# Kernel tuning notes

Hardware: AMD Instinct MI355X
Metric: run time of the kernel (lower is better)

Reference implementation:

```python
import jax, jax.numpy as jnp
import numpy as np

VOCAB, EMBED, HID = 10, 256, 512
B, S, T = 8, 1024, 256  # Senc = S // 4 = 256


def _conv1d(x, w, b):
    # x: (B, Cin, L), w: (Cout, Cin, 3), padding=1 -> same length
    y = jax.lax.conv_general_dilated(x, w, window_strides=(1,), padding=[(1, 1)],
                                     dimension_numbers=('NCH', 'OIH', 'NCH'))
    return y + b[None, :, None]


def _maxpool2(x):
    # MaxPool1d(kernel=2, stride=2) on (B, C, L)
    b, c, l = x.shape
    return x.reshape(b, c, l // 2, 2).max(axis=-1)


def _lstm_layer(x, wih, whh, bih, bhh):
    # x: (B, T, Din); PyTorch gate order i, f, g, o; zero initial state
    b, t, _ = x.shape
    h_dim = whh.shape[1]
    xg = x @ wih.T + (bih + bhh)  # (B, T, 4H) - input projection hoisted out of scan

    def step(carry, xt):
        h, c = carry
        gates = xt + h @ whh.T
        i, f, g, o = jnp.split(gates, 4, axis=-1)
        c = jax.nn.sigmoid(f) * c + jax.nn.sigmoid(i) * jnp.tanh(g)
        h = jax.nn.sigmoid(o) * jnp.tanh(c)
        return (h, c), h

    init = (jnp.zeros((b, h_dim), x.dtype), jnp.zeros((b, h_dim), x.dtype))
    _, hs = jax.lax.scan(step, init, jnp.swapaxes(xg, 0, 1))
    return jnp.swapaxes(hs, 0, 1)  # (B, T, H)


def setup_inputs() -> dict:
    key = jax.random.key(0)
    ks = jax.random.split(key, 24)

    def unif(k, shape, fan_in):
        bound = 1.0 / np.sqrt(fan_in)
        return jax.random.uniform(k, shape, jnp.float32, -bound, bound)

    inp = {
        'src': jax.random.randint(ks[0], (B, S), 0, VOCAB),
        'tgt': jax.random.randint(ks[1], (B, T), 0, VOCAB),
        'embedding': jax.random.normal(ks[2], (VOCAB, EMBED), jnp.float32),
        'conv1_w': unif(ks[3], (256, EMBED, 3), EMBED * 3),
        'conv1_b': unif(ks[4], (256,), EMBED * 3),
        'conv2_w': unif(ks[5], (512, 256, 3), 256 * 3),
        'conv2_b': unif(ks[6], (512,), 256 * 3),
        'conv3_w': unif(ks[7], (512, 512, 3), 512 * 3),
        'conv3_b': unif(ks[8], (512,), 512 * 3),
        'lstm0_wih': unif(ks[9], (4 * HID, EMBED), HID),
        'lstm0_whh': unif(ks[10], (4 * HID, HID), HID),
        'lstm0_bih': unif(ks[11], (4 * HID,), HID),
        'lstm0_bhh': unif(ks[12], (4 * HID,), HID),
        'lstm1_wih': unif(ks[13], (4 * HID, HID), HID),
        'lstm1_whh': unif(ks[14], (4 * HID, HID), HID),
        'lstm1_bih': unif(ks[15], (4 * HID,), HID),
        'lstm1_bhh': unif(ks[16], (4 * HID,), HID),
        'attn_w': unif(ks[17], (1, 2 * HID), 2 * HID),
        'attn_b': unif(ks[18], (1,), 2 * HID),
        'out_w': unif(ks[19], (VOCAB, HID), HID),
        'out_b': unif(ks[20], (VOCAB,), HID),
    }
    return inp


def reference(src, tgt, embedding, conv1_w, conv1_b, conv2_w, conv2_b, conv3_w, conv3_b,
              lstm0_wih, lstm0_whh, lstm0_bih, lstm0_bhh,
              lstm1_wih, lstm1_whh, lstm1_bih, lstm1_bhh,
              attn_w, attn_b, out_w, out_b):
    # --- CNN encoder ---
    x = jnp.swapaxes(embedding[src], 1, 2)          # (B, E, S)
    x = _maxpool2(jax.nn.relu(_conv1d(x, conv1_w, conv1_b)))
    x = _maxpool2(jax.nn.relu(_conv1d(x, conv2_w, conv2_b)))
    x = jax.nn.relu(_conv1d(x, conv3_w, conv3_b))
    enc = jnp.swapaxes(x, 1, 2)                     # (B, Senc, 512)

    # --- LSTM decoder (2 layers) ---
    h = _lstm_layer(embedding[tgt], lstm0_wih, lstm0_whh, lstm0_bih, lstm0_bhh)
    dec = _lstm_layer(h, lstm1_wih, lstm1_whh, lstm1_bih, lstm1_bhh)  # (B, T, 512)

    # --- Bahdanau-style attention ---
    # Linear(cat([dec, enc])) == dec @ W[:, :H].T + enc @ W[:, H:].T + b,
    # so broadcast the two rank-1 projections instead of materializing (B,T,Senc,1024).
    dec_p = jnp.einsum('bth,h->bt', dec, attn_w[0, :HID])   # (B, T)
    enc_p = jnp.einsum('bsh,h->bs', enc, attn_w[0, HID:])   # (B, Senc)
    scores = dec_p[:, :, None] + enc_p[:, None, :] + attn_b[0]  # (B, T, Senc)
    attn = jax.nn.softmax(scores, axis=2)
    context = jnp.einsum('bts,bsd->btd', attn, enc)         # (B, T, 512)

    output = dec @ out_w.T + out_b                          # (B, T, VOCAB)
    # Original module computes context then discards it; we return it too so the
    # attention workload is not dead-code-eliminated under jit.
    return output, context
```

## Files before the change

kernel.cpp:

```cpp
#include <hip/hip_runtime.h>
#include <cstddef>

constexpr int OXB0 = 0;
constexpr int OXB1 = OXB0 + 8 * 1026 * 256;
constexpr int OXB2 = OXB1 + 8 * 514 * 256;
constexpr int OENC = OXB2 + 8 * 258 * 512;
constexpr int OWR1 = OENC + 8 * 256 * 512;
constexpr int OWR2 = OWR1 + 768 * 256;
constexpr int OWR3 = OWR2 + 768 * 512;
constexpr int OWR0 = OWR3 + 1536 * 512;
constexpr int OTGT = OWR0 + 256 * 2048;
constexpr int OXG0 = OTGT + 2048 * 256;
constexpr int OH0S = OXG0 + 2048 * 2048;
constexpr int OH1S = OH0S + 257 * 4096;
constexpr int OCTX = OH1S + 257 * 4096;
constexpr int OFLG = OCTX + 8 * 512;

constexpr int FSTR = 16;

__device__ __forceinline__ float hsum4(const float4& a) { return a.x + a.y + a.z + a.w; }
__device__ __forceinline__ float4 relu4(float4 v, const float4& bv) {
    v.x = fmaxf(v.x + bv.x, 0.f); v.y = fmaxf(v.y + bv.y, 0.f);
    v.z = fmaxf(v.z + bv.z, 0.f); v.w = fmaxf(v.w + bv.w, 0.f); return v;
}
__device__ __forceinline__ float4 max4(const float4& a, const float4& b) {
    float4 r; r.x = fmaxf(a.x, b.x); r.y = fmaxf(a.y, b.y);
    r.z = fmaxf(a.z, b.z); r.w = fmaxf(a.w, b.w); return r;
}
__device__ __forceinline__ float sigmf(float x) { return 1.f / (1.f + expf(-x)); }
__device__ __forceinline__ void fma4(float4& acc, const float4& a, const float4& b) {
    acc.x = fmaf(a.x, b.x, acc.x); acc.y = fmaf(a.y, b.y, acc.y);
    acc.z = fmaf(a.z, b.z, acc.z); acc.w = fmaf(a.w, b.w, acc.w);
}

__device__ __forceinline__ unsigned long long aload64(const float* p) {
    return __hip_atomic_load((const unsigned long long*)p, __ATOMIC_RELAXED,
                             __HIP_MEMORY_SCOPE_AGENT);
}
__device__ __forceinline__ void astore32(float* p, float v) {
    __hip_atomic_store((unsigned int*)p, __float_as_uint(v), __ATOMIC_RELAXED,
                       __HIP_MEMORY_SCOPE_AGENT);
}
__device__ __forceinline__ int aloadi(const int* p) {
    return __hip_atomic_load(p, __ATOMIC_RELAXED, __HIP_MEMORY_SCOPE_AGENT);
}
__device__ __forceinline__ void astorei(int* p, int v) {
    __hip_atomic_store(p, v, __ATOMIC_RELAXED, __HIP_MEMORY_SCOPE_AGENT);
}
__device__ __forceinline__ float2 unpack64(unsigned long long v) {
    float2 f;
    f.x = __uint_as_float((unsigned)v);
    f.y = __uint_as_float((unsigned)(v >> 32));
    return f;
}

__global__ void init_kernel(float* __restrict__ ws, int* __restrict__ flags) {
    int idx = blockIdx.x * 256 + threadIdx.x;
    int stride = gridDim.x * 256;
    for (int i = idx; i < 257 * 4096; i += stride) {
        ws[OH0S + i] = 0.f;
        ws[OH1S + i] = 0.f;
    }
    for (int i = idx; i < 192 * FSTR; i += stride) flags[i] = 0;
    for (int i = idx; i < 8 * 2 * 256; i += stride) {
        int b = i >> 9, rr = (i >> 8) & 1, c = i & 255;
        ws[OXB1 + b * 131584 + (rr ? 513 : 0) * 256 + c] = 0.f;
    }
    for (int i = idx; i < 8 * 2 * 512; i += stride) {
        int b = i >> 10, rr = (i >> 9) & 1, c = i & 511;
        ws[OXB2 + b * 132096 + (rr ? 257 : 0) * 512 + c] = 0.f;
    }
}

__global__ void embed_src_kernel(const int* __restrict__ src, const float* __restrict__ emb,
                                 float* __restrict__ xb0) {
    int fi = blockIdx.x * 256 + threadIdx.x;
    int e4 = fi & 63;
    int r = fi >> 6;
    int b = r / 1026;
    int p = r - b * 1026;
    float4 v = make_float4(0.f, 0.f, 0.f, 0.f);
    if (p > 0 && p < 1025) {
        int row = src[b * 1024 + (p - 1)];
        v = *(const float4*)(emb + row * 256 + e4 * 4);
    }
    *(float4*)(xb0 + (size_t)fi * 4) = v;
}

__global__ void gather_tgt_kernel(const int* __restrict__ tgt, const float* __restrict__ emb,
                                  float* __restrict__ et) {
    int fi = blockIdx.x * 256 + threadIdx.x;
    int e4 = fi & 63;
    int r = fi >> 6;
    int t = r >> 3, b = r & 7;
    int row = tgt[b * 256 + t];
    *(float4*)(et + (size_t)fi * 4) = *(const float4*)(emb + row * 256 + e4 * 4);
}

__global__ void tr_conv_kernel(const float* __restrict__ w, float* __restrict__ wr,
                               int Cout, int Cin) {
    int idx = blockIdx.x * 256 + threadIdx.x;
    int co = idx / (Cin * 3);
    int rem = idx - co * Cin * 3;
    int ci = rem / 3;
    int dk = rem - ci * 3;
    wr[(dk * Cin + ci) * Cout + co] = w[idx];
}
__global__ void tr_mat_kernel(const float* __restrict__ w, float* __restrict__ wr,
                              int N, int K) {
    int idx = blockIdx.x * 256 + threadIdx.x;
    int n = idx / K;
    int k = idx - n * K;
    wr[k * N + n] = w[idx];
}

__launch_bounds__(256)
// ... 37 lines not shown
            acc0.x = fmaf(a4.x, b4.x, acc0.x); acc0.y = fmaf(a4.x, b4.y, acc0.y);
            acc0.z = fmaf(a4.x, b4.z, acc0.z); acc0.w = fmaf(a4.x, b4.w, acc0.w);
            acc1.x = fmaf(a4.y, b4.x, acc1.x); acc1.y = fmaf(a4.y, b4.y, acc1.y);
            acc1.z = fmaf(a4.y, b4.z, acc1.z); acc1.w = fmaf(a4.y, b4.w, acc1.w);
            acc2.x = fmaf(a4.z, b4.x, acc2.x); acc2.y = fmaf(a4.z, b4.y, acc2.y);
            acc2.z = fmaf(a4.z, b4.z, acc2.z); acc2.w = fmaf(a4.z, b4.w, acc2.w);
            acc3.x = fmaf(a4.w, b4.x, acc3.x); acc3.y = fmaf(a4.w, b4.y, acc3.y);
            acc3.z = fmaf(a4.w, b4.z, acc3.z); acc3.w = fmaf(a4.w, b4.w, acc3.w);
        }
        __syncthreads();
    }

    int nb = n0 + tco * 4;
    float4 bv;
    bv.x = bias[nb + 0]; bv.y = bias[nb + 1]; bv.z = bias[nb + 2]; bv.w = bias[nb + 3];
    if (bias2) { bv.x += bias2[nb + 0]; bv.y += bias2[nb + 1]; bv.z += bias2[nb + 2]; bv.w += bias2[nb + 3]; }

    if (mode == 0) {
        float4 v0 = acc0, v1 = acc1, v2 = acc2, v3 = acc3;
        v0.x += bv.x; v0.y += bv.y; v0.z += bv.z; v0.w += bv.w;
        v1.x += bv.x; v1.y += bv.y; v1.z += bv.z; v1.w += bv.w;
        v2.x += bv.x; v2.y += bv.y; v2.z += bv.z; v2.w += bv.w;
        v3.x += bv.x; v3.y += bv.y; v3.z += bv.z; v3.w += bv.w;
        int mr = m0 + tl * 4;
        *(float4*)(out + (size_t)(mr + 0) * N + nb) = v0;
        *(float4*)(out + (size_t)(mr + 1) * N + nb) = v1;
        *(float4*)(out + (size_t)(mr + 2) * N + nb) = v2;
        *(float4*)(out + (size_t)(mr + 3) * N + nb) = v3;
    } else if (mode == 1) {
        float4 v0 = relu4(acc0, bv), v1 = relu4(acc1, bv), v2 = relu4(acc2, bv), v3 = relu4(acc3, bv);
        float4 p0 = max4(v0, v1), p1 = max4(v2, v3);
        int lout = (m0 + tl * 4) >> 1;
        float* ob = out + (size_t)b * oBS + (size_t)(1 + lout) * N + nb;
        *(float4*)ob = p0;
        *(float4*)(ob + N) = p1;
    } else {
        float4 v0 = relu4(acc0, bv), v1 = relu4(acc1, bv), v2 = relu4(acc2, bv), v3 = relu4(acc3, bv);
        int mr = m0 + tl * 4;
        float* ob = out + (size_t)b * oBS + (size_t)mr * N + nb;
        *(float4*)(ob + 0 * N) = v0;
        *(float4*)(ob + 1 * N) = v1;
        *(float4*)(ob + 2 * N) = v2;
        *(float4*)(ob + 3 * N) = v3;
    }
}

__launch_bounds__(256, 1)
__global__ void lstm_kernel(const float* __restrict__ xg0,
                            const float* __restrict__ whh0,
                            const float* __restrict__ wih1,
                            const float* __restrict__ whh1,
                            const float* __restrict__ bih1,
                            const float* __restrict__ bhh1,
                            float* __restrict__ h0s, float* __restrict__ h1s,
                            int* __restrict__ flags) {
    const int tid = threadIdx.x;
    const int wg = blockIdx.x;

    if (wg < 64) {
        const int wg0 = wg;
        const int cg = tid >> 6;
        const int bg = (tid >> 5) & 1;
        const int ks = tid & 31;
        float2 W2[4][2][8];
#pragma unroll
        for (int g = 0; g < 4; ++g)
#pragma unroll
            for (int e = 0; e < 2; ++e) {
                const float* wr = whh0 + (size_t)(g * 512 + wg0 * 8 + cg * 2 + e) * 512 + ks * 2;
#pragma unroll
                for (int q = 0; q < 8; ++q)
                    W2[g][e][q] = *(const float2*)(wr + q * 64);
            }
        const int vg = ks >> 3, ve = (ks >> 2) & 1, vbi = ks & 3;
        const int vb = bg * 4 + vbi;
        const size_t xgoff = (size_t)vb * 2048 + vg * 512 + wg0 * 8 + cg * 2 + ve;
        const int ob = bg * 4 + (ks & 3);
        const int ou = cg * 2 + ((ks >> 2) & 1);
        float cst = 0.f;

        for (int t = 0; t < 256; ++t) {
            float xgv = xg0[(size_t)t * 16384 + xgoff];
            if (t > 0 && tid < 64) {
                int gd = 1 << 20;
                while (aloadi(&flags[tid * FSTR]) < t && --gd) {}
            }
            __syncthreads();
            unsigned long long hv[4][8];
#pragma unroll
            for (int bi = 0; bi < 4; ++bi) {
                const float* hb = h0s + (size_t)t * 4096 + (bg * 4 + bi) * 512 + ks * 2;
#pragma unroll
                for (int q = 0; q < 8; ++q)
                    hv[bi][q] = aload64(hb + q * 64);
            }
            float2 acc[4][2][4];
#pragma unroll
            for (int g = 0; g < 4; ++g)
#pragma unroll
                for (int e = 0; e < 2; ++e)
#pragma unroll
                    for (int bi = 0; bi < 4; ++bi) acc[g][e][bi] = make_float2(0.f, 0.f);
#pragma unroll
            for (int q = 0; q < 8; ++q)
#pragma unroll
                for (int bi = 0; bi < 4; ++bi) {
                    float2 h2 = unpack64(hv[bi][q]);
#pragma unroll
                    for (int g = 0; g < 4; ++g)
#pragma unroll
                        for (int e = 0; e < 2; ++e) {
                            acc[g][e][bi].x = fmaf(W2[g][e][q].x, h2.x, acc[g][e][bi].x);
                            acc[g][e][bi].y = fmaf(W2[g][e][q].y, h2.y, acc[g][e][bi].y);
                        }
                }
            float s[32];
#pragma unroll
            for (int g = 0; g < 4; ++g)
#pragma unroll
                for (int e = 0; e < 2; ++e)
#pragma unroll
                    for (int bi = 0; bi < 4; ++bi)
                        s[g * 8 + e * 4 + bi] = acc[g][e][bi].x + acc[g][e][bi].y;
#pragma unroll
            for (int i = 0; i < 16; ++i) {
                float t_ = (ks & 16) ? s[i] : s[i + 16];
                float k_ = (ks & 16) ? s[i + 16] : s[i];
                s[i] = k_ + __shfl_xor(t_, 16);
            }
#pragma unroll
            for (int i = 0; i < 8; ++i) {
                float t_ = (ks & 8) ? s[i] : s[i + 8];
                float k_ = (ks & 8) ? s[i + 8] : s[i];
                s[i] = k_ + __shfl_xor(t_, 8);
            }
#pragma unroll
            for (int i = 0; i < 4; ++i) {
                float t_ = (ks & 4) ? s[i] : s[i + 4];
                float k_ = (ks & 4) ? s[i + 4] : s[i];
                s[i] = k_ + __shfl_xor(t_, 4);
            }
#pragma unroll
            for (int i = 0; i < 2; ++i) {
                float t_ = (ks & 2) ? s[i] : s[i + 2];
                float k_ = (ks & 2) ? s[i + 2] : s[i];
                s[i] = k_ + __shfl_xor(t_, 2);
            }
            {
                float t_ = (ks & 1) ? s[0] : s[1];
                float k_ = (ks & 1) ? s[1] : s[0];
                s[0] = k_ + __shfl_xor(t_, 1);
            }
            float red = s[0] + xgv;
            float fgv = __shfl_xor(red, 8);
            float ggv = __shfl_xor(red, 16);
            float ogv = __shfl_xor(red, 24);
            if (ks < 8) {
                cst = sigmf(fgv) * cst + sigmf(red) * tanhf(ggv);
                float hval = sigmf(ogv) * tanhf(cst);
                astore32(h0s + (size_t)(t + 1) * 4096 + ob * 512 + wg0 * 8 + ou, hval);
            }
            asm volatile("s_waitcnt vmcnt(0)" ::: "memory");
            __syncthreads();
            if (tid == 0) astorei(&flags[wg0 * FSTR], t + 1);
        }
    } else {
        const int wg1 = wg - 64;
        const int w = tid >> 6;
        const int cg = w >> 1, bgv = w & 1;
        const int ks = tid & 63;
        float2 W2[4][2][8];
#pragma unroll
        for (int g = 0; g < 4; ++g)
#pragma unroll
            for (int e = 0; e < 2; ++e) {
                const size_t ro = (size_t)(g * 512 + wg1 * 4 + cg * 2 + e) * 512 + ks * 2;
#pragma unroll
                for (int q = 0; q < 4; ++q)
                    W2[g][e][q] = *(const float2*)(wih1 + ro + q * 128);
#pragma unroll
                for (int q = 4; q < 8; ++q)
                    W2[g][e][q] = *(const float2*)(whh1 + ro + (q - 4) * 128);
            }
        const int vg = (((ks >> 5) & 1) << 1) | ((ks >> 3) & 1);
        const int ve = (ks >> 2) & 1, vbi = ks & 3;
        const int rv = vg * 512 + wg1 * 4 + cg * 2 + ve;
        const float biasv = bih1[rv] + bhh1[rv];
        const int ob = bgv * 4 + (ks & 3);
        const int ou = cg * 2 + ((ks >> 2) & 1);
        float cst = 0.f;

        for (int t = 0; t < 256; ++t) {
            if (tid < 64) {
                int gd = 1 << 20;
                while (aloadi(&flags[tid * FSTR]) < t + 1 && --gd) {}
            } else if (tid < 192 && t > 0) {
                int gd = 1 << 20;
                while (aloadi(&flags[tid * FSTR]) < t && --gd) {}
            }
            __syncthreads();
            unsigned long long hv[4][8];
#pragma unroll
            for (int bi = 0; bi < 4; ++bi) {
                const float* h0b = h0s + (size_t)(t + 1) * 4096 + (bgv * 4 + bi) * 512 + ks * 2;
                const float* h1b = h1s + (size_t)t * 4096 + (bgv * 4 + bi) * 512 + ks * 2;
#pragma unroll
                for (int q = 0; q < 4; ++q) hv[bi][q] = aload64(h0b + q * 128);
#pragma unroll
                for (int q = 4; q < 8; ++q) hv[bi][q] = aload64(h1b + (q - 4) * 128);
            }
            float2 acc[4][2][4];
#pragma unroll
            for (int g = 0; g < 4; ++g)
#pragma unroll
                for (int e = 0; e < 2; ++e)
#pragma unroll
                    for (int bi = 0; bi < 4; ++bi) acc[g][e][bi] = make_float2(0.f, 0.f);
#pragma unroll
            for (int q = 0; q < 8; ++q)
#pragma unroll
                for (int bi = 0; bi < 4; ++bi) {
                    float2 h2 = unpack64(hv[bi][q]);
#pragma unroll
                    for (int g = 0; g < 4; ++g)
#pragma unroll
                        for (int e = 0; e < 2; ++e) {
                            acc[g][e][bi].x = fmaf(W2[g][e][q].x, h2.x, acc[g][e][bi].x);
                            acc[g][e][bi].y = fmaf(W2[g][e][q].y, h2.y, acc[g][e][bi].y);
                        }
                }
            float s[32];
#pragma unroll
            for (int g = 0; g < 4; ++g)
#pragma unroll
                for (int e = 0; e < 2; ++e)
#pragma unroll
                    for (int bi = 0; bi < 4; ++bi)
                        s[g * 8 + e * 4 + bi] = acc[g][e][bi].x + acc[g][e][bi].y;
#pragma unroll
            for (int i = 0; i < 16; ++i) {
                float t_ = (ks & 32) ? s[i] : s[i + 16];
                float k_ = (ks & 32) ? s[i + 16] : s[i];
                s[i] = k_ + __shfl_xor(t_, 32);
            }
#pragma unroll
            for (int i = 0; i < 8; ++i) {
                float t_ = (ks & 8) ? s[i] : s[i + 8];
                float k_ = (ks & 8) ? s[i + 8] : s[i];
                s[i] = k_ + __shfl_xor(t_, 8);
            }
#pragma unroll
            for (int i = 0; i < 4; ++i) {
                float t_ = (ks & 4) ? s[i] : s[i + 4];
                float k_ = (ks & 4) ? s[i + 4] : s[i];
                s[i] = k_ + __shfl_xor(t_, 4);
            }
#pragma unroll
            for (int i = 0; i < 2; ++i) {
                float t_ = (ks & 2) ? s[i] : s[i + 2];
                float k_ = (ks & 2) ? s[i + 2] : s[i];
                s[i] = k_ + __shfl_xor(t_, 2);
            }
            {
                float t_ = (ks & 1) ? s[0] : s[1];
                float k_ = (ks & 1) ? s[1] : s[0];
                s[0] = k_ + __shfl_xor(t_, 1);
            }
            s[0] += __shfl_xor(s[0], 16);
            float red = s[0] + biasv;
            float fgv = __shfl_xor(red, 8);
            float ggv = __shfl_xor(red, 32);
            float ogv = __shfl_xor(red, 40);
            if (ks < 8) {
                cst = sigmf(fgv) * cst + sigmf(red) * tanhf(ggv);
                float hval = sigmf(ogv) * tanhf(cst);
                astore32(h1s + (size_t)(t + 1) * 4096 + ob * 512 + wg1 * 4 + ou, hval);
            }
            asm volatile("s_waitcnt vmcnt(0)" ::: "memory");
            __syncthreads();
            if (tid == 0) astorei(&flags[(64 + wg1) * FSTR], t + 1);
        }
    }
}

__launch_bounds__(256)
__global__ void attn_kernel(const float* __restrict__ enc, const float* __restrict__ attn_w,
                            float* __restrict__ ctx) {
    __shared__ float aw[512];
    __shared__ float pr[256];
    __shared__ float red[8];
    const int b = blockIdx.x, tid = threadIdx.x;
    if (tid < 128) ((float4*)aw)[tid] = ((const float4*)(attn_w + 512))[tid];
    __syncthreads();
    const float* er = enc + (size_t)(b * 256 + tid) * 512;
    float4 a4 = make_float4(0, 0, 0, 0);
#pragma unroll 8
    for (int i = 0; i < 128; ++i) {
        float4 e4 = *(const float4*)(er + i * 4);
        float4 w4 = *(const float4*)(aw + i * 4);
        fma4(a4, e4, w4);
    }
    float v = hsum4(a4);
    float m = v;
#pragma unroll
    for (int off = 32; off > 0; off >>= 1) m = fmaxf(m, __shfl_xor(m, off));
    if ((tid & 63) == 0) red[tid >> 6] = m;
    __syncthreads();
    if (tid == 0) red[4] = fmaxf(fmaxf(red[0], red[1]), fmaxf(red[2], red[3]));
    __syncthreads();
    float e = expf(v - red[4]);
    pr[tid] = e;
    float s = e;
#pragma unroll
    for (int off = 32; off > 0; off >>= 1) s += __shfl_xor(s, off);
    if ((tid & 63) == 0) red[tid >> 6] = s;
    __syncthreads();
    if (tid == 0) red[5] = red[0] + red[1] + red[2] + red[3];
    __syncthreads();
    float inv = 1.f / red[5];
    for (int hh = tid; hh < 512; hh += 256) {
        float acc = 0.f;
#pragma unroll 8
        for (int s2 = 0; s2 < 256; ++s2)
            acc = fmaf(pr[s2], enc[(size_t)(b * 256 + s2) * 512 + hh], acc);
        ctx[b * 512 + hh] = acc * inv;
    }
}

__global__ void bcast_ctx_kernel(const float* __restrict__ ctx, float* __restrict__ outc) {
    int fi = blockIdx.x * 256 + threadIdx.x;
    int h4 = fi & 127;
    int b = fi >> 15;
    ((float4*)outc)[fi] = ((const float4*)ctx)[b * 128 + h4];
// ... 15 lines not shown
        float4 w0 = *(const float4*)wr, w1 = *(const float4*)(wr + 4);
        acc[v] = d0.x * w0.x + d0.y * w0.y + d0.z * w0.z + d0.w * w0.w +
                 d1.x * w1.x + d1.y * w1.y + d1.z * w1.z + d1.w * w1.w;
    }
#pragma unroll
    for (int v = 0; v < 10; ++v)
#pragma unroll
        for (int off = 32; off > 0; off >>= 1) acc[v] += __shfl_xor(acc[v], off);
    if (lane == 0) {
        float* o = out + (size_t)(b * 256 + t) * 10;
#pragma unroll
        for (int v = 0; v < 10; ++v) o[v] = acc[v] + ob[v];
    }
}

extern "C" void kernel_launch(void* const* d_in, const int* in_sizes, int n_in,
                              void* d_out, int out_size, void* d_ws, size_t ws_size,
                              hipStream_t stream) {
    const int* src = (const int*)d_in[0];
    const int* tgt = (const int*)d_in[1];
    const float* emb = (const float*)d_in[2];
    const float* c1w = (const float*)d_in[3];
    const float* c1b = (const float*)d_in[4];
    const float* c2w = (const float*)d_in[5];
    const float* c2b = (const float*)d_in[6];
    const float* c3w = (const float*)d_in[7];
    const float* c3b = (const float*)d_in[8];
    const float* wih0 = (const float*)d_in[9];
    const float* whh0 = (const float*)d_in[10];
    const float* bih0 = (const float*)d_in[11];
    const float* bhh0 = (const float*)d_in[12];
    const float* wih1 = (const float*)d_in[13];
    const float* whh1 = (const float*)d_in[14];
    const float* bih1 = (const float*)d_in[15];
    const float* bhh1 = (const float*)d_in[16];
    const float* attn_w = (const float*)d_in[17];
    const float* out_w = (const float*)d_in[19];
    const float* out_b = (const float*)d_in[20];

    float* ws = (float*)d_ws;
    float* xb0 = ws + OXB0;
    float* xb1 = ws + OXB1;
    float* xb2 = ws + OXB2;
    float* enc = ws + OENC;
    float* wr1 = ws + OWR1;
    float* wr2 = ws + OWR2;
    float* wr3 = ws + OWR3;
    float* wr0 = ws + OWR0;
    float* etg = ws + OTGT;
    float* xg0 = ws + OXG0;
    float* h0s = ws + OH0S;
    float* h1s = ws + OH1S;
    float* ctx = ws + OCTX;
    int* flags = (int*)(ws + OFLG);
    float* outp = (float*)d_out;

    init_kernel<<<1024, 256, 0, stream>>>(ws, flags);
    embed_src_kernel<<<2052, 256, 0, stream>>>(src, emb, xb0);
    gather_tgt_kernel<<<512, 256, 0, stream>>>(tgt, emb, etg);
    tr_conv_kernel<<<768, 256, 0, stream>>>(c1w, wr1, 256, 256);
    tr_conv_kernel<<<1536, 256, 0, stream>>>(c2w, wr2, 512, 256);
    tr_conv_kernel<<<3072, 256, 0, stream>>>(c3w, wr3, 512, 512);
    tr_mat_kernel<<<2048, 256, 0, stream>>>(wih0, wr0, 2048, 256);

    gemm_kernel<<<dim3(32, 32, 1), 256, 0, stream>>>(etg, 0, 256, 256, wr0, 2048,
                                                     bih0, bhh0, xg0, 0, 0);
    gemm_kernel<<<dim3(16, 4, 8), 256, 0, stream>>>(xb0, 262656, 256, 768, wr1, 256,
                                                    c1b, nullptr, xb1, 131584, 1);
    gemm_kernel<<<dim3(8, 8, 8), 256, 0, stream>>>(xb1, 131584, 256, 768, wr2, 512,
                                                   c2b, nullptr, xb2, 132096, 1);
    gemm_kernel<<<dim3(4, 8, 8), 256, 0, stream>>>(xb2, 132096, 512, 1536, wr3, 512,
                                                   c3b, nullptr, enc, 131072, 2);
    lstm_kernel<<<192, 256, 0, stream>>>(xg0, whh0, wih1, whh1, bih1, bhh1,
                                         h0s, h1s, flags);
    attn_kernel<<<8, 256, 0, stream>>>(enc, attn_w, ctx);
    bcast_ctx_kernel<<<1024, 256, 0, stream>>>(ctx, outp + 20480);
    out_proj_kernel<<<512, 256, 0, stream>>>(h1s, out_w, out_b, outp);
}
```

Baseline: 1.434 ms.

## Replace LSTM flag barriers with sentinel-valued hidden-state polling

The persistent LSTM kernel no longer uses per-workgroup step flags plus __syncthreads. Hidden-state buffers are instead pre-filled with a NaN sentinel, and each wave spins reading its own h inputs until no sentinel remains. Each wave consumes data as soon as it arrives, which removes the flag round-trip and the block-wide barriers from the serial recurrence. Outputs are also written as paired 64-bit atomic stores. The risk is that correctness relies on the sentinel never appearing as a real value and on the 64-bit stores being atomic; the polling also re-reads all h loads, adding memory traffic.

```diff
diff --git a/kernel.cpp b/kernel.cpp
--- a/kernel.cpp
+++ b/kernel.cpp
@@ -14,9 +14,8 @@
 constexpr int OH0S = OXG0 + 2048 * 2048;
 constexpr int OH1S = OH0S + 257 * 4096;
 constexpr int OCTX = OH1S + 257 * 4096;
-constexpr int OFLG = OCTX + 8 * 512;
-
-constexpr int FSTR = 16;
+
+constexpr unsigned SENT = 0x7FC0DEADu;
 
 __device__ __forceinline__ float hsum4(const float4& a) { return a.x + a.y + a.z + a.w; }
 __device__ __forceinline__ float4 relu4(float4 v, const float4& bv) {
@@ -37,15 +36,11 @@
     return __hip_atomic_load((const unsigned long long*)p, __ATOMIC_RELAXED,
                              __HIP_MEMORY_SCOPE_AGENT);
 }
-__device__ __forceinline__ void astore32(float* p, float v) {
-    __hip_atomic_store((unsigned int*)p, __float_as_uint(v), __ATOMIC_RELAXED,
+__device__ __forceinline__ void astore64(float* p, float lo, float hi) {
+    unsigned long long v = ((unsigned long long)__float_as_uint(hi) << 32) |
+                           (unsigned long long)__float_as_uint(lo);
+    __hip_atomic_store((unsigned long long*)p, v, __ATOMIC_RELAXED,
                        __HIP_MEMORY_SCOPE_AGENT);
-}
-__device__ __forceinline__ int aloadi(const int* p) {
-    return __hip_atomic_load(p, __ATOMIC_RELAXED, __HIP_MEMORY_SCOPE_AGENT);
-}
-__device__ __forceinline__ void astorei(int* p, int v) {
-    __hip_atomic_store(p, v, __ATOMIC_RELAXED, __HIP_MEMORY_SCOPE_AGENT);
 }
 __device__ __forceinline__ float2 unpack64(unsigned long long v) {
     float2 f;
@@ -54,14 +49,15 @@
     return f;
 }
 
-__global__ void init_kernel(float* __restrict__ ws, int* __restrict__ flags) {
+__global__ void init_kernel(float* __restrict__ ws) {
     int idx = blockIdx.x * 256 + threadIdx.x;
     int stride = gridDim.x * 256;
+    float sentf = __uint_as_float(SENT);
     for (int i = idx; i < 257 * 4096; i += stride) {
-        ws[OH0S + i] = 0.f;
-        ws[OH1S + i] = 0.f;
-    }
-    for (int i = idx; i < 192 * FSTR; i += stride) flags[i] = 0;
+        float v = (i < 4096) ? 0.f : sentf;
+        ws[OH0S + i] = v;
+        ws[OH1S + i] = v;
+    }
     for (int i = idx; i < 8 * 2 * 256; i += stride) {
         int b = i >> 9, rr = (i >> 8) & 1, c = i & 255;
         ws[OXB1 + b * 131584 + (rr ? 513 : 0) * 256 + c] = 0.f;
@@ -205,8 +201,7 @@
                             const float* __restrict__ whh1,
                             const float* __restrict__ bih1,
                             const float* __restrict__ bhh1,
-                            float* __restrict__ h0s, float* __restrict__ h1s,
-                            int* __restrict__ flags) {
+                            float* __restrict__ h0s, float* __restrict__ h1s) {
     const int tid = threadIdx.x;
     const int wg = blockIdx.x;
 
@@ -229,23 +224,29 @@
         const int vb = bg * 4 + vbi;
         const size_t xgoff = (size_t)vb * 2048 + vg * 512 + wg0 * 8 + cg * 2 + ve;
         const int ob = bg * 4 + (ks & 3);
-        const int ou = cg * 2 + ((ks >> 2) & 1);
         float cst = 0.f;
 
         for (int t = 0; t < 256; ++t) {
             float xgv = xg0[(size_t)t * 16384 + xgoff];
-            if (t > 0 && tid < 64) {
-                int gd = 1 << 20;
-                while (aloadi(&flags[tid * FSTR]) < t && --gd) {}
-            }
-            __syncthreads();
             unsigned long long hv[4][8];
-#pragma unroll
-            for (int bi = 0; bi < 4; ++bi) {
-                const float* hb = h0s + (size_t)t * 4096 + (bg * 4 + bi) * 512 + ks * 2;
-#pragma unroll
-                for (int q = 0; q < 8; ++q)
-                    hv[bi][q] = aload64(hb + q * 64);
+            int gd = 1 << 20;
+            for (;;) {
+#pragma unroll
+                for (int bi = 0; bi < 4; ++bi) {
+                    const float* hb = h0s + (size_t)t * 4096 + (bg * 4 + bi) * 512 + ks * 2;
+#pragma unroll
+                    for (int q = 0; q < 8; ++q)
+                        hv[bi][q] = aload64(hb + q * 64);
+                }
+                unsigned bad = 0;
+#pragma unroll
+                for (int bi = 0; bi < 4; ++bi)
+#pragma unroll
+                    for (int q = 0; q < 8; ++q) {
+                        unsigned long long v = hv[bi][q];
+                        bad |= ((unsigned)v == SENT) | ((unsigned)(v >> 32) == SENT);
+                    }
+                if (!__any((int)bad) || --gd <= 0) break;
             }
             float2 acc[4][2][4];
 #pragma unroll
@@ -308,14 +309,13 @@
             float fgv = __shfl_xor(red, 8);
             float ggv = __shfl_xor(red, 16);
             float ogv = __shfl_xor(red, 24);
-            if (ks < 8) {
-                cst = sigmf(fgv) * cst + sigmf(red) * tanhf(ggv);
-                float hval = sigmf(ogv) * tanhf(cst);
-                astore32(h0s + (size_t)(t + 1) * 4096 + ob * 512 + wg0 * 8 + ou, hval);
-            }
+            cst = sigmf(fgv) * cst + sigmf(red) * tanhf(ggv);
+            float hval = sigmf(ogv) * tanhf(cst);
+            float hval_e1 = __shfl_xor(hval, 4);
+            if (ks < 4)
+                astore64(h0s + (size_t)(t + 1) * 4096 + ob * 512 + wg0 * 8 + cg * 2,
+                         hval, hval_e1);
             asm volatile("s_waitcnt vmcnt(0)" ::: "memory");
-            __syncthreads();
-            if (tid == 0) astorei(&flags[wg0 * FSTR], t + 1);
         }
     } else {
         const int wg1 = wg - 64;
@@ -340,27 +340,30 @@
         const int rv = vg * 512 + wg1 * 4 + cg * 2 + ve;
         const float biasv = bih1[rv] + bhh1[rv];
         const int ob = bgv * 4 + (ks & 3);
-        const int ou = cg * 2 + ((ks >> 2) & 1);
         float cst = 0.f;
 
         for (int t = 0; t < 256; ++t) {
-            if (tid < 64) {
-                int gd = 1 << 20;
-                while (aloadi(&flags[tid * FSTR]) < t + 1 && --gd) {}
-            } else if (tid < 192 && t > 0) {
-                int gd = 1 << 20;
-                while (aloadi(&flags[tid * FSTR]) < t && --gd) {}
-            }
-            __syncthreads();
             unsigned long long hv[4][8];
-#pragma unroll
-            for (int bi = 0; bi < 4; ++bi) {
-                const float* h0b = h0s + (size_t)(t + 1) * 4096 + (bgv * 4 + bi) * 512 + ks * 2;
-                const float* h1b = h1s + (size_t)t * 4096 + (bgv * 4 + bi) * 512 + ks * 2;
-#pragma unroll
-                for (int q = 0; q < 4; ++q) hv[bi][q] = aload64(h0b + q * 128);
-#pragma unroll
-                for (int q = 4; q < 8; ++q) hv[bi][q] = aload64(h1b + (q - 4) * 128);
+            int gd = 1 << 20;
+            for (;;) {
+#pragma unroll
+                for (int bi = 0; bi < 4; ++bi) {
+                    const float* h0b = h0s + (size_t)(t + 1) * 4096 + (bgv * 4 + bi) * 512 + ks * 2;
+                    const float* h1b = h1s + (size_t)t * 4096 + (bgv * 4 + bi) * 512 + ks * 2;
+#pragma unroll
+                    for (int q = 0; q < 4; ++q) hv[bi][q] = aload64(h0b + q * 128);
+#pragma unroll
+                    for (int q = 4; q < 8; ++q) hv[bi][q] = aload64(h1b + (q - 4) * 128);
+                }
+                unsigned bad = 0;
+#pragma unroll
+                for (int bi = 0; bi < 4; ++bi)
+#pragma unroll
+                    for (int q = 0; q < 8; ++q) {
+                        unsigned long long v = hv[bi][q];
+                        bad |= ((unsigned)v == SENT) | ((unsigned)(v >> 32) == SENT);
+                    }
+                if (!__any((int)bad) || --gd <= 0) break;
             }
             float2 acc[4][2][4];
 #pragma unroll
@@ -424,14 +427,13 @@
             float fgv = __shfl_xor(red, 8);
             float ggv = __shfl_xor(red, 32);
             float ogv = __shfl_xor(red, 40);
-            if (ks < 8) {
-                cst = sigmf(fgv) * cst + sigmf(red) * tanhf(ggv);
-                float hval = sigmf(ogv) * tanhf(cst);
-                astore32(h1s + (size_t)(t + 1) * 4096 + ob * 512 + wg1 * 4 + ou, hval);
-            }
+            cst = sigmf(fgv) * cst + sigmf(red) * tanhf(ggv);
+            float hval = sigmf(ogv) * tanhf(cst);
+            float hval_e1 = __shfl_xor(hval, 4);
+            if (ks < 4)
+                astore64(h1s + (size_t)(t + 1) * 4096 + ob * 512 + wg1 * 4 + cg * 2,
+                         hval, hval_e1);
             asm volatile("s_waitcnt vmcnt(0)" ::: "memory");
-            __syncthreads();
-            if (tid == 0) astorei(&flags[(64 + wg1) * FSTR], t + 1);
         }
     }
 }
@@ -553,10 +555,9 @@
     float* h0s = ws + OH0S;
     float* h1s = ws + OH1S;
     float* ctx = ws + OCTX;
-    int* flags = (int*)(ws + OFLG);
     float* outp = (float*)d_out;
 
-    init_kernel<<<1024, 256, 0, stream>>>(ws, flags);
+    init_kernel<<<1024, 256, 0, stream>>>(ws);
     embed_src_kernel<<<2052, 256, 0, stream>>>(src, emb, xb0);
     gather_tgt_kernel<<<512, 256, 0, stream>>>(tgt, emb, etg);
     tr_conv_kernel<<<768, 256, 0, stream>>>(c1w, wr1, 256, 256);
@@ -573,7 +574,7 @@
     gemm_kernel<<<dim3(4, 8, 8), 256, 0, stream>>>(xb2, 132096, 512, 1536, wr3, 512,
                                                    c3b, nullptr, enc, 131072, 2);
     lstm_kernel<<<192, 256, 0, stream>>>(xg0, whh0, wih1, whh1, bih1, bhh1,
-                                         h0s, h1s, flags);
+                                         h0s, h1s);
     attn_kernel<<<8, 256, 0, stream>>>(enc, attn_w, ctx);
     bcast_ctx_kernel<<<1024, 256, 0, stream>>>(ctx, outp + 20480);
     out_proj_kernel<<<512, 256, 0, stream>>>(h1s, out_w, out_b, outp);
```

Result: slower. 2.324 ms (+62.1%).

## Halve LSTM workgroups by processing two unit slices per block, shrinking flag polling

Applied to the files above, without the earlier changes.

The persistent LSTM kernel now runs 96 workgroups instead of 192. Each block keeps two weight slices in registers and computes two hidden-unit groups per timestep, so the hidden-state loads are shared and fewer flags have to be polled at each inter-block barrier. The flags are packed densely instead of padded to 16 ints. The init kernel also zeroes only the initial h state rather than the whole history buffer. In exchange, each block carries twice as many weight registers and does twice the serial compute per step, which lengthens the critical path of every step and risks register spills.

```diff
diff --git a/kernel.cpp b/kernel.cpp
--- a/kernel.cpp
+++ b/kernel.cpp
@@ -16,9 +16,7 @@
 constexpr int OCTX = OH1S + 257 * 4096;
 constexpr int OFLG = OCTX + 8 * 512;
 
-constexpr int FSTR = 16;
-
-__device__ __forceinline__ float hsum4(const float4& a) { return a.x + a.y + a.z + a.w; }
+__device__ __forceinline__ float sigmf(float x) { return 1.f / (1.f + expf(-x)); }
 __device__ __forceinline__ float4 relu4(float4 v, const float4& bv) {
     v.x = fmaxf(v.x + bv.x, 0.f); v.y = fmaxf(v.y + bv.y, 0.f);
     v.z = fmaxf(v.z + bv.z, 0.f); v.w = fmaxf(v.w + bv.w, 0.f); return v;
@@ -27,11 +25,11 @@
     float4 r; r.x = fmaxf(a.x, b.x); r.y = fmaxf(a.y, b.y);
     r.z = fmaxf(a.z, b.z); r.w = fmaxf(a.w, b.w); return r;
 }
-__device__ __forceinline__ float sigmf(float x) { return 1.f / (1.f + expf(-x)); }
 __device__ __forceinline__ void fma4(float4& acc, const float4& a, const float4& b) {
     acc.x = fmaf(a.x, b.x, acc.x); acc.y = fmaf(a.y, b.y, acc.y);
     acc.z = fmaf(a.z, b.z, acc.z); acc.w = fmaf(a.w, b.w, acc.w);
 }
+__device__ __forceinline__ float hsum4(const float4& a) { return a.x + a.y + a.z + a.w; }
 
 __device__ __forceinline__ unsigned long long aload64(const float* p) {
     return __hip_atomic_load((const unsigned long long*)p, __ATOMIC_RELAXED,
@@ -54,14 +52,159 @@
     return f;
 }
 
+__device__ __forceinline__ void l0_half(const float2 (&W)[4][2][8],
+                                        const unsigned long long (&hv)[4][8],
+                                        float xgv, float& cst, int ks,
+                                        float* outp) {
+    float2 acc[4][2][4];
+#pragma unroll
+    for (int g = 0; g < 4; ++g)
+#pragma unroll
+        for (int e = 0; e < 2; ++e)
+#pragma unroll
+            for (int bi = 0; bi < 4; ++bi) acc[g][e][bi] = make_float2(0.f, 0.f);
+#pragma unroll
+    for (int q = 0; q < 8; ++q)
+#pragma unroll
+        for (int bi = 0; bi < 4; ++bi) {
+            float2 h2 = unpack64(hv[bi][q]);
+#pragma unroll
+            for (int g = 0; g < 4; ++g)
+#pragma unroll
+                for (int e = 0; e < 2; ++e) {
+                    acc[g][e][bi].x = fmaf(W[g][e][q].x, h2.x, acc[g][e][bi].x);
+                    acc[g][e][bi].y = fmaf(W[g][e][q].y, h2.y, acc[g][e][bi].y);
+                }
+        }
+    float s[32];
+#pragma unroll
+    for (int g = 0; g < 4; ++g)
+#pragma unroll
+        for (int e = 0; e < 2; ++e)
+#pragma unroll
+            for (int bi = 0; bi < 4; ++bi)
+                s[g * 8 + e * 4 + bi] = acc[g][e][bi].x + acc[g][e][bi].y;
+#pragma unroll
+    for (int i = 0; i < 16; ++i) {
+        float t_ = (ks & 16) ? s[i] : s[i + 16];
+        float k_ = (ks & 16) ? s[i + 16] : s[i];
+        s[i] = k_ + __shfl_xor(t_, 16);
+    }
+#pragma unroll
+    for (int i = 0; i < 8; ++i) {
+        float t_ = (ks & 8) ? s[i] : s[i + 8];
+        float k_ = (ks & 8) ? s[i + 8] : s[i];
+        s[i] = k_ + __shfl_xor(t_, 8);
+    }
+#pragma unroll
+    for (int i = 0; i < 4; ++i) {
+        float t_ = (ks & 4) ? s[i] : s[i + 4];
+        float k_ = (ks & 4) ? s[i + 4] : s[i];
+        s[i] = k_ + __shfl_xor(t_, 4);
+    }
+#pragma unroll
+    for (int i = 0; i < 2; ++i) {
+        float t_ = (ks & 2) ? s[i] : s[i + 2];
+        float k_ = (ks & 2) ? s[i + 2] : s[i];
+        s[i] = k_ + __shfl_xor(t_, 2);
+    }
+    {
+        float t_ = (ks & 1) ? s[0] : s[1];
+        float k_ = (ks & 1) ? s[1] : s[0];
+        s[0] = k_ + __shfl_xor(t_, 1);
+    }
+    float red = s[0] + xgv;
+    float fgv = __shfl_xor(red, 8);
+    float ggv = __shfl_xor(red, 16);
+    float ogv = __shfl_xor(red, 24);
+    if (ks < 8) {
+        cst = sigmf(fgv) * cst + sigmf(red) * tanhf(ggv);
+        float hval = sigmf(ogv) * tanhf(cst);
+        astore32(outp, hval);
+    }
+}
+
+__device__ __forceinline__ void l1_half(const float2 (&W)[4][2][8],
+                                        const unsigned long long (&hv)[4][8],
+                                        float biasv, float& cst, int ks,
+                                        float* outp) {
+    float2 acc[4][2][4];
+#pragma unroll
+    for (int g = 0; g < 4; ++g)
+#pragma unroll
+        for (int e = 0; e < 2; ++e)
+#pragma unroll
+            for (int bi = 0; bi < 4; ++bi) acc[g][e][bi] = make_float2(0.f, 0.f);
+#pragma unroll
+    for (int q = 0; q < 8; ++q)
+#pragma unroll
+        for (int bi = 0; bi < 4; ++bi) {
+            float2 h2 = unpack64(hv[bi][q]);
+#pragma unroll
+            for (int g = 0; g < 4; ++g)
+#pragma unroll
+                for (int e = 0; e < 2; ++e) {
+                    acc[g][e][bi].x = fmaf(W[g][e][q].x, h2.x, acc[g][e][bi].x);
+                    acc[g][e][bi].y = fmaf(W[g][e][q].y, h2.y, acc[g][e][bi].y);
+                }
+        }
+    float s[32];
+#pragma unroll
+    for (int g = 0; g < 4; ++g)
+#pragma unroll
+        for (int e = 0; e < 2; ++e)
+#pragma unroll
+            for (int bi = 0; bi < 4; ++bi)
+                s[g * 8 + e * 4 + bi] = acc[g][e][bi].x + acc[g][e][bi].y;
+#pragma unroll
+    for (int i = 0; i < 16; ++i) {
+        float t_ = (ks & 32) ? s[i] : s[i + 16];
+        float k_ = (ks & 32) ? s[i + 16] : s[i];
+        s[i] = k_ + __shfl_xor(t_, 32);
+    }
+#pragma unroll
+    for (int i = 0; i < 8; ++i) {
+        float t_ = (ks & 8) ? s[i] : s[i + 8];
+        float k_ = (ks & 8) ? s[i + 8] : s[i];
+        s[i] = k_ + __shfl_xor(t_, 8);
+    }
+#pragma unroll
+    for (int i = 0; i < 4; ++i) {
+        float t_ = (ks & 4) ? s[i] : s[i + 4];
+        float k_ = (ks & 4) ? s[i + 4] : s[i];
+        s[i] = k_ + __shfl_xor(t_, 4);
+    }
+#pragma unroll
+    for (int i = 0; i < 2; ++i) {
+        float t_ = (ks & 2) ? s[i] : s[i + 2];
+        float k_ = (ks & 2) ? s[i + 2] : s[i];
+        s[i] = k_ + __shfl_xor(t_, 2);
+    }
+    {
+        float t_ = (ks & 1) ? s[0] : s[1];
+        float k_ = (ks & 1) ? s[1] : s[0];
+        s[0] = k_ + __shfl_xor(t_, 1);
+    }
+    s[0] += __shfl_xor(s[0], 16);
+    float red = s[0] + biasv;
+    float fgv = __shfl_xor(red, 8);
+    float ggv = __shfl_xor(red, 32);
+    float ogv = __shfl_xor(red, 40);
+    if (ks < 8) {
+        cst = sigmf(fgv) * cst + sigmf(red) * tanhf(ggv);
+        float hval = sigmf(ogv) * tanhf(cst);
+        astore32(outp, hval);
+    }
+}
+
 __global__ void init_kernel(float* __restrict__ ws, int* __restrict__ flags) {
     int idx = blockIdx.x * 256 + threadIdx.x;
     int stride = gridDim.x * 256;
-    for (int i = idx; i < 257 * 4096; i += stride) {
+    for (int i = idx; i < 4096; i += stride) {
         ws[OH0S + i] = 0.f;
         ws[OH1S + i] = 0.f;
     }
-    for (int i = idx; i < 192 * FSTR; i += stride) flags[i] = 0;
+    for (int i = idx; i < 96; i += stride) flags[i] = 0;
     for (int i = idx; i < 8 * 2 * 256; i += stride) {
         int b = i >> 9, rr = (i >> 8) & 1, c = i & 255;
         ws[OXB1 + b * 131584 + (rr ? 513 : 0) * 256 + c] = 0.f;
@@ -210,33 +353,41 @@
     const int tid = threadIdx.x;
     const int wg = blockIdx.x;
 
-    if (wg < 64) {
+    if (wg < 32) {
         const int wg0 = wg;
         const int cg = tid >> 6;
         const int bg = (tid >> 5) & 1;
         const int ks = tid & 31;
-        float2 W2[4][2][8];
+        const int e0A = wg0 * 2, e0B = wg0 * 2 + 1;
+        float2 WA[4][2][8], WB[4][2][8];
 #pragma unroll
         for (int g = 0; g < 4; ++g)
 #pragma unroll
             for (int e = 0; e < 2; ++e) {
-                const float* wr = whh0 + (size_t)(g * 512 + wg0 * 8 + cg * 2 + e) * 512 + ks * 2;
-#pragma unroll
-                for (int q = 0; q < 8; ++q)
-                    W2[g][e][q] = *(const float2*)(wr + q * 64);
+                const float* wrA = whh0 + (size_t)(g * 512 + e0A * 8 + cg * 2 + e) * 512 + ks * 2;
+                const float* wrB = whh0 + (size_t)(g * 512 + e0B * 8 + cg * 2 + e) * 512 + ks * 2;
+#pragma unroll
+                for (int q = 0; q < 8; ++q) {
+                    WA[g][e][q] = *(const float2*)(wrA + q * 64);
+                    WB[g][e][q] = *(const float2*)(wrB + q * 64);
+                }
             }
         const int vg = ks >> 3, ve = (ks >> 2) & 1, vbi = ks & 3;
         const int vb = bg * 4 + vbi;
-        const size_t xgoff = (size_t)vb * 2048 + vg * 512 + wg0 * 8 + cg * 2 + ve;
+        const size_t xgoffA = (size_t)vb * 2048 + vg * 512 + e0A * 8 + cg * 2 + ve;
+        const size_t xgoffB = (size_t)vb * 2048 + vg * 512 + e0B * 8 + cg * 2 + ve;
         const int ob = bg * 4 + (ks & 3);
         const int ou = cg * 2 + ((ks >> 2) & 1);
-        float cst = 0.f;
+        const size_t obaseA = (size_t)ob * 512 + e0A * 8 + ou;
+        const size_t obaseB = (size_t)ob * 512 + e0B * 8 + ou;
+        float cstA = 0.f, cstB = 0.f;
 
         for (int t = 0; t < 256; ++t) {
-            float xgv = xg0[(size_t)t * 16384 + xgoff];
-            if (t > 0 && tid < 64) {
+            float xgvA = xg0[(size_t)t * 16384 + xgoffA];
+            float xgvB = xg0[(size_t)t * 16384 + xgoffB];
+            if (t > 0 && tid < 32) {
                 int gd = 1 << 20;
-                while (aloadi(&flags[tid * FSTR]) < t && --gd) {}
+                while (aloadi(&flags[tid]) < t && --gd) {}
             }
             __syncthreads();
             unsigned long long hv[4][8];
@@ -247,109 +398,56 @@
                 for (int q = 0; q < 8; ++q)
                     hv[bi][q] = aload64(hb + q * 64);
             }
-            float2 acc[4][2][4];
-#pragma unroll
-            for (int g = 0; g < 4; ++g)
-#pragma unroll
-                for (int e = 0; e < 2; ++e)
-#pragma unroll
-                    for (int bi = 0; bi < 4; ++bi) acc[g][e][bi] = make_float2(0.f, 0.f);
-#pragma unroll
-            for (int q = 0; q < 8; ++q)
-#pragma unroll
-                for (int bi = 0; bi < 4; ++bi) {
-                    float2 h2 = unpack64(hv[bi][q]);
-#pragma unroll
-                    for (int g = 0; g < 4; ++g)
-#pragma unroll
-                        for (int e = 0; e < 2; ++e) {
-                            acc[g][e][bi].x = fmaf(W2[g][e][q].x, h2.x, acc[g][e][bi].x);
-                            acc[g][e][bi].y = fmaf(W2[g][e][q].y, h2.y, acc[g][e][bi].y);
-                        }
-                }
-            float s[32];
-#pragma unroll
-            for (int g = 0; g < 4; ++g)
-#pragma unroll
-                for (int e = 0; e < 2; ++e)
-#pragma unroll
-                    for (int bi = 0; bi < 4; ++bi)
-                        s[g * 8 + e * 4 + bi] = acc[g][e][bi].x + acc[g][e][bi].y;
-#pragma unroll
-            for (int i = 0; i < 16; ++i) {
-                float t_ = (ks & 16) ? s[i] : s[i + 16];
-                float k_ = (ks & 16) ? s[i + 16] : s[i];
-                s[i] = k_ + __shfl_xor(t_, 16);
-            }
-#pragma unroll
-            for (int i = 0; i < 8; ++i) {
-                float t_ = (ks & 8) ? s[i] : s[i + 8];
-                float k_ = (ks & 8) ? s[i + 8] : s[i];
-                s[i] = k_ + __shfl_xor(t_, 8);
-            }
-#pragma unroll
-            for (int i = 0; i < 4; ++i) {
-                float t_ = (ks & 4) ? s[i] : s[i + 4];
-                float k_ = (ks & 4) ? s[i + 4] : s[i];
-                s[i] = k_ + __shfl_xor(t_, 4);
-            }
-#pragma unroll
-            for (int i = 0; i < 2; ++i) {
-                float t_ = (ks & 2) ? s[i] : s[i + 2];
-                float k_ = (ks & 2) ? s[i + 2] : s[i];
-                s[i] = k_ + __shfl_xor(t_, 2);
-            }
-            {
-                float t_ = (ks & 1) ? s[0] : s[1];
-                float k_ = (ks & 1) ? s[1] : s[0];
-                s[0] = k_ + __shfl_xor(t_, 1);
-            }
-            float red = s[0] + xgv;
-            float fgv = __shfl_xor(red, 8);
-            float ggv = __shfl_xor(red, 16);
-            float ogv = __shfl_xor(red, 24);
-            if (ks < 8) {
-                cst = sigmf(fgv) * cst + sigmf(red) * tanhf(ggv);
-                float hval = sigmf(ogv) * tanhf(cst);
-                astore32(h0s + (size_t)(t + 1) * 4096 + ob * 512 + wg0 * 8 + ou, hval);
-            }
+            float* pl = h0s + (size_t)(t + 1) * 4096;
+            l0_half(WA, hv, xgvA, cstA, ks, pl + obaseA);
+            l0_half(WB, hv, xgvB, cstB, ks, pl + obaseB);
             asm volatile("s_waitcnt vmcnt(0)" ::: "memory");
             __syncthreads();
-            if (tid == 0) astorei(&flags[wg0 * FSTR], t + 1);
+            if (tid == 0) astorei(&flags[wg0], t + 1);
         }
     } else {
-        const int wg1 = wg - 64;
+        const int wg1 = wg - 32;
         const int w = tid >> 6;
         const int cg = w >> 1, bgv = w & 1;
         const int ks = tid & 63;
-        float2 W2[4][2][8];
+        const int e1A = wg1 * 2, e1B = wg1 * 2 + 1;
+        float2 WA[4][2][8], WB[4][2][8];
 #pragma unroll
         for (int g = 0; g < 4; ++g)
 #pragma unroll
             for (int e = 0; e < 2; ++e) {
-                const size_t ro = (size_t)(g * 512 + wg1 * 4 + cg * 2 + e) * 512 + ks * 2;
-#pragma unroll
-                for (int q = 0; q < 4; ++q)
-                    W2[g][e][q] = *(const float2*)(wih1 + ro + q * 128);
-#pragma unroll
-                for (int q = 4; q < 8; ++q)
-                    W2[g][e][q] = *(const float2*)(whh1 + ro + (q - 4) * 128);
+                const size_t roA = (size_t)(g * 512 + e1A * 4 + cg * 2 + e) * 512 + ks * 2;
+                const size_t roB = (size_t)(g * 512 + e1B * 4 + cg * 2 + e) * 512 + ks * 2;
+#pragma unroll
+                for (int q = 0; q < 4; ++q) {
+                    WA[g][e][q] = *(const float2*)(wih1 + roA + q * 128);
+                    WB[g][e][q] = *(const float2*)(wih1 + roB + q * 128);
+                }
+#pragma unroll
+                for (int q = 4; q < 8; ++q) {
+                    WA[g][e][q] = *(const float2*)(whh1 + roA + (q - 4) * 128);
+                    WB[g][e][q] = *(const float2*)(whh1 + roB + (q - 4) * 128);
+                }
             }
         const int vg = (((ks >> 5) & 1) << 1) | ((ks >> 3) & 1);
-        const int ve = (ks >> 2) & 1, vbi = ks & 3;
-        const int rv = vg * 512 + wg1 * 4 + cg * 2 + ve;
-        const float biasv = bih1[rv] + bhh1[rv];
+        const int ve = (ks >> 2) & 1;
+        const int rvA = vg * 512 + e1A * 4 + cg * 2 + ve;
+        const int rvB = vg * 512 + e1B * 4 + cg * 2 + ve;
+        const float biasA = bih1[rvA] + bhh1[rvA];
+        const float biasB = bih1[rvB] + bhh1[rvB];
         const int ob = bgv * 4 + (ks & 3);
         const int ou = cg * 2 + ((ks >> 2) & 1);
-        float cst = 0.f;
+        const size_t obaseA = (size_t)ob * 512 + e1A * 4 + ou;
+        const size_t obaseB = (size_t)ob * 512 + e1B * 4 + ou;
+        float cstA = 0.f, cstB = 0.f;
 
         for (int t = 0; t < 256; ++t) {
-            if (tid < 64) {
+            if (tid < 32) {
                 int gd = 1 << 20;
-                while (aloadi(&flags[tid * FSTR]) < t + 1 && --gd) {}
-            } else if (tid < 192 && t > 0) {
+                while (aloadi(&flags[tid]) < t + 1 && --gd) {}
+            } else if (tid >= 64 && tid < 128 && t > 0) {
                 int gd = 1 << 20;
-                while (aloadi(&flags[tid * FSTR]) < t && --gd) {}
+                while (aloadi(&flags[32 + tid - 64]) < t && --gd) {}
             }
             __syncthreads();
             unsigned long long hv[4][8];
@@ -362,76 +460,12 @@
 #pragma unroll
                 for (int q = 4; q < 8; ++q) hv[bi][q] = aload64(h1b + (q - 4) * 128);
             }
-            float2 acc[4][2][4];
-#pragma unroll
-            for (int g = 0; g < 4; ++g)
-#pragma unroll
-                for (int e = 0; e < 2; ++e)
-#pragma unroll
-                    for (int bi = 0; bi < 4; ++bi) acc[g][e][bi] = make_float2(0.f, 0.f);
-#pragma unroll
-            for (int q = 0; q < 8; ++q)
-#pragma unroll
-                for (int bi = 0; bi < 4; ++bi) {
-                    float2 h2 = unpack64(hv[bi][q]);
-#pragma unroll
-                    for (int g = 0; g < 4; ++g)
-#pragma unroll
-                        for (int e = 0; e < 2; ++e) {
-                            acc[g][e][bi].x = fmaf(W2[g][e][q].x, h2.x, acc[g][e][bi].x);
-                            acc[g][e][bi].y = fmaf(W2[g][e][q].y, h2.y, acc[g][e][bi].y);
-                        }
-                }
-            float s[32];
-#pragma unroll
-            for (int g = 0; g < 4; ++g)
-#pragma unroll
-                for (int e = 0; e < 2; ++e)
-#pragma unroll
-                    for (int bi = 0; bi < 4; ++bi)
-                        s[g * 8 + e * 4 + bi] = acc[g][e][bi].x + acc[g][e][bi].y;
-#pragma unroll
-            for (int i = 0; i < 16; ++i) {
-                float t_ = (ks & 32) ? s[i] : s[i + 16];
-                float k_ = (ks & 32) ? s[i + 16] : s[i];
-                s[i] = k_ + __shfl_xor(t_, 32);
-            }
-#pragma unroll
-            for (int i = 0; i < 8; ++i) {
-                float t_ = (ks & 8) ? s[i] : s[i + 8];
-                float k_ = (ks & 8) ? s[i + 8] : s[i];
-                s[i] = k_ + __shfl_xor(t_, 8);
-            }
-#pragma unroll
-            for (int i = 0; i < 4; ++i) {
-                float t_ = (ks & 4) ? s[i] : s[i + 4];
-                float k_ = (ks & 4) ? s[i + 4] : s[i];
-                s[i] = k_ + __shfl_xor(t_, 4);
-            }
-#pragma unroll
-            for (int i = 0; i < 2; ++i) {
-                float t_ = (ks & 2) ? s[i] : s[i + 2];
-                float k_ = (ks & 2) ? s[i + 2] : s[i];
-                s[i] = k_ + __shfl_xor(t_, 2);
-            }
-            {
-                float t_ = (ks & 1) ? s[0] : s[1];
-                float k_ = (ks & 1) ? s[1] : s[0];
-                s[0] = k_ + __shfl_xor(t_, 1);
-            }
-            s[0] += __shfl_xor(s[0], 16);
-            float red = s[0] + biasv;
-            float fgv = __shfl_xor(red, 8);
-            float ggv = __shfl_xor(red, 32);
-            float ogv = __shfl_xor(red, 40);
-            if (ks < 8) {
-                cst = sigmf(fgv) * cst + sigmf(red) * tanhf(ggv);
-                float hval = sigmf(ogv) * tanhf(cst);
-                astore32(h1s + (size_t)(t + 1) * 4096 + ob * 512 + wg1 * 4 + ou, hval);
-            }
+            float* pl = h1s + (size_t)(t + 1) * 4096;
+            l1_half(WA, hv, biasA, cstA, ks, pl + obaseA);
+            l1_half(WB, hv, biasB, cstB, ks, pl + obaseB);
             asm volatile("s_waitcnt vmcnt(0)" ::: "memory");
             __syncthreads();
-            if (tid == 0) astorei(&flags[(64 + wg1) * FSTR], t + 1);
+            if (tid == 0) astorei(&flags[32 + wg1], t + 1);
         }
     }
 }
@@ -572,8 +606,8 @@
                                                    c2b, nullptr, xb2, 132096, 1);
     gemm_kernel<<<dim3(4, 8, 8), 256, 0, stream>>>(xb2, 132096, 512, 1536, wr3, 512,
                                                    c3b, nullptr, enc, 131072, 2);
-    lstm_kernel<<<192, 256, 0, stream>>>(xg0, whh0, wih1, whh1, bih1, bhh1,
-                                         h0s, h1s, flags);
+    lstm_kernel<<<96, 256, 0, stream>>>(xg0, whh0, wih1, whh1, bih1, bhh1,
+                                        h0s, h1s, flags);
     attn_kernel<<<8, 256, 0, stream>>>(enc, attn_w, ctx);
     bcast_ctx_kernel<<<1024, 256, 0, stream>>>(ctx, outp + 20480);
     out_proj_kernel<<<512, 256, 0, stream>>>(h1s, out_w, out_b, outp);
```

Measured after the change: 2.280 ms. +59.0%, slower.

## Validate hidden-state loads with NaN sentinels instead of draining stores before flag

Applied to the files above, without the earlier changes.

The hidden-state history buffers are now pre-filled with a sentinel NaN pattern for every step after the first. Consumers re-read their h slice until no sentinel remains, and producers no longer wait for their stores to drain before bumping the progress flag. The aim is to shorten the per-step critical path of the persistent LSTM recurrence by taking the store-drain wait off it. The cost is retry loads and extra compares per step, and ordering now depends on data validity rather than the flag alone.

```diff
diff --git a/kernel.cpp b/kernel.cpp
--- a/kernel.cpp
+++ b/kernel.cpp
@@ -17,6 +17,7 @@
 constexpr int OFLG = OCTX + 8 * 512;
 
 constexpr int FSTR = 16;
+constexpr unsigned SENT = 0x7FC0DEADu;
 
 __device__ __forceinline__ float hsum4(const float4& a) { return a.x + a.y + a.z + a.w; }
 __device__ __forceinline__ float4 relu4(float4 v, const float4& bv) {
@@ -53,13 +54,18 @@
     f.y = __uint_as_float((unsigned)(v >> 32));
     return f;
 }
+__device__ __forceinline__ unsigned sent_in(unsigned long long v) {
+    return ((unsigned)v == SENT) | ((unsigned)(v >> 32) == SENT);
+}
 
 __global__ void init_kernel(float* __restrict__ ws, int* __restrict__ flags) {
     int idx = blockIdx.x * 256 + threadIdx.x;
     int stride = gridDim.x * 256;
+    float sentf = __uint_as_float(SENT);
     for (int i = idx; i < 257 * 4096; i += stride) {
-        ws[OH0S + i] = 0.f;
-        ws[OH1S + i] = 0.f;
+        float v = (i < 4096) ? 0.f : sentf;
+        ws[OH0S + i] = v;
+        ws[OH1S + i] = v;
     }
     for (int i = idx; i < 192 * FSTR; i += stride) flags[i] = 0;
     for (int i = idx; i < 8 * 2 * 256; i += stride) {
@@ -240,12 +246,21 @@
             }
             __syncthreads();
             unsigned long long hv[4][8];
-#pragma unroll
-            for (int bi = 0; bi < 4; ++bi) {
-                const float* hb = h0s + (size_t)t * 4096 + (bg * 4 + bi) * 512 + ks * 2;
-#pragma unroll
-                for (int q = 0; q < 8; ++q)
-                    hv[bi][q] = aload64(hb + q * 64);
+            int gd = 1 << 16;
+            for (;;) {
+#pragma unroll
+                for (int bi = 0; bi < 4; ++bi) {
+                    const float* hb = h0s + (size_t)t * 4096 + (bg * 4 + bi) * 512 + ks * 2;
+#pragma unroll
+                    for (int q = 0; q < 8; ++q)
+                        hv[bi][q] = aload64(hb + q * 64);
+                }
+                unsigned bad = 0;
+#pragma unroll
+                for (int bi = 0; bi < 4; ++bi)
+#pragma unroll
+                    for (int q = 0; q < 8; ++q) bad |= sent_in(hv[bi][q]);
+                if (!__any((int)bad) || --gd <= 0) break;
             }
             float2 acc[4][2][4];
 #pragma unroll
@@ -313,7 +328,6 @@
                 float hval = sigmf(ogv) * tanhf(cst);
                 astore32(h0s + (size_t)(t + 1) * 4096 + ob * 512 + wg0 * 8 + ou, hval);
             }
-            asm volatile("s_waitcnt vmcnt(0)" ::: "memory");
             __syncthreads();
             if (tid == 0) astorei(&flags[wg0 * FSTR], t + 1);
         }
@@ -353,14 +367,23 @@
             }
             __syncthreads();
             unsigned long long hv[4][8];
-#pragma unroll
-            for (int bi = 0; bi < 4; ++bi) {
-                const float* h0b = h0s + (size_t)(t + 1) * 4096 + (bgv * 4 + bi) * 512 + ks * 2;
-                const float* h1b = h1s + (size_t)t * 4096 + (bgv * 4 + bi) * 512 + ks * 2;
-#pragma unroll
-                for (int q = 0; q < 4; ++q) hv[bi][q] = aload64(h0b + q * 128);
-#pragma unroll
-                for (int q = 4; q < 8; ++q) hv[bi][q] = aload64(h1b + (q - 4) * 128);
+            int gd = 1 << 16;
+            for (;;) {
+#pragma unroll
+                for (int bi = 0; bi < 4; ++bi) {
+                    const float* h0b = h0s + (size_t)(t + 1) * 4096 + (bgv * 4 + bi) * 512 + ks * 2;
+                    const float* h1b = h1s + (size_t)t * 4096 + (bgv * 4 + bi) * 512 + ks * 2;
+#pragma unroll
+                    for (int q = 0; q < 4; ++q) hv[bi][q] = aload64(h0b + q * 128);
+#pragma unroll
+                    for (int q = 4; q < 8; ++q) hv[bi][q] = aload64(h1b + (q - 4) * 128);
+                }
+                unsigned bad = 0;
+#pragma unroll
+                for (int bi = 0; bi < 4; ++bi)
+#pragma unroll
+                    for (int q = 0; q < 8; ++q) bad |= sent_in(hv[bi][q]);
+                if (!__any((int)bad) || --gd <= 0) break;
             }
             float2 acc[4][2][4];
 #pragma unroll
@@ -429,7 +452,6 @@
                 float hval = sigmf(ogv) * tanhf(cst);
                 astore32(h1s + (size_t)(t + 1) * 4096 + ob * 512 + wg1 * 4 + ou, hval);
             }
-            asm volatile("s_waitcnt vmcnt(0)" ::: "memory");
             __syncthreads();
             if (tid == 0) astorei(&flags[(64 + wg1) * FSTR], t + 1);
         }
```

Result: no change. 1.414 ms (-1.4%).
